# Kernel tuning notes

Hardware: AMD Instinct MI355X
Metric: run time of the kernel (lower is better)

The kernel has to match this reference:

```python
import jax, jax.numpy as jnp
import numpy as np

HEADS = 16
LN_EPS = 1e-5


def setup_inputs() -> dict:
    key = jax.random.key(0)
    ks = jax.random.split(key, 8)
    B, S, D = 2, 2048, 1024
    F = 4 * D
    std = 0.02
    return {
        "x": jax.random.normal(ks[0], (B, S, D), jnp.float32),
        # QKV projections (stored as (in, out)); kaiming-normal-like scale
        "Wq": jax.random.normal(ks[1], (D, D), jnp.float32) * std,
        "bq": jnp.zeros((D,), jnp.float32),
        "Wk": jax.random.normal(ks[2], (D, D), jnp.float32) * std,
        "bk": jnp.zeros((D,), jnp.float32),
        "Wv": jax.random.normal(ks[3], (D, D), jnp.float32) * std,
        "bv": jnp.zeros((D,), jnp.float32),
        # FFN
        "W1": jax.random.normal(ks[4], (D, F), jnp.float32) * std,
        "b1": jnp.zeros((F,), jnp.float32),
        "W2": jax.random.normal(ks[5], (F, D), jnp.float32) * std,
        "b2": jnp.zeros((D,), jnp.float32),
        # LayerNorm
        "gamma": jnp.ones((D,), jnp.float32),
        "beta": jnp.zeros((D,), jnp.float32),
    }


def reference(x, Wq, bq, Wk, bk, Wv, bv, W1, b1, W2, b2, gamma, beta):
    B, S, D = x.shape
    H = HEADS
    hd = D // H
    # QKV projections -> [B, H, S, hd]
    Q = (x @ Wq + bq).reshape(B, S, H, hd).transpose(0, 2, 1, 3)
    K = (x @ Wk + bk).reshape(B, S, H, hd).transpose(0, 2, 1, 3)
    V = (x @ Wv + bv).reshape(B, S, H, hd).transpose(0, 2, 1, 3)
    # scores scaled by sqrt(embedding_dim), faithful to source (not head_dim)
    scores = jnp.einsum('bhqd,bhkd->bhqk', Q, K) / jnp.sqrt(jnp.asarray(D, x.dtype))
    attn = jax.nn.softmax(scores, axis=-1)
    # diagonal_training: zero the diagonal of the post-softmax attention matrix
    attn = attn * (1.0 - jnp.eye(S, dtype=attn.dtype))
    out = jnp.einsum('bhqk,bhkd->bhqd', attn, V)
    out = out.transpose(0, 2, 1, 3).reshape(B, S, D)
    # dropout is identity in eval mode
    h = jax.nn.gelu(out @ W1 + b1, approximate=False) @ W2 + b2
    # LayerNorm
    mu = jnp.mean(h, axis=-1, keepdims=True)
    var = jnp.var(h, axis=-1, keepdims=True)
    return (h - mu) * jax.lax.rsqrt(var + LN_EPS) * gamma + beta
```

## Files before the change

kernel.cpp:

```cpp
#include <hip/hip_runtime.h>

using bf16x8 = __attribute__((ext_vector_type(8))) short;
using f32x4  = __attribute__((ext_vector_type(4))) float;

__device__ __forceinline__ float b2f(ushort u) {
  union { unsigned int i; float f; } v; v.i = ((unsigned int)u) << 16; return v.f;
}
__device__ __forceinline__ ushort f2b(float f) {
  unsigned int x = __float_as_uint(f);
  unsigned int r = (x + 0x7FFFu + ((x >> 16) & 1u)) >> 16;
  return (ushort)r;
}
__device__ __forceinline__ unsigned cvt_pk_bf16(float a, float b) {
  unsigned r;
  asm("v_cvt_pk_bf16_f32 %0, %1, %2" : "=v"(r) : "v"(a), "v"(b));
  return r;
}

__device__ __forceinline__ void gld_lds16(const void* g, void* l) {
  __builtin_amdgcn_global_load_lds(
      (const __attribute__((address_space(1))) void*)g,
      (__attribute__((address_space(3))) void*)l, 16, 0, 0);
}


__global__ void cast_bf16_kernel(const float* __restrict__ in, ushort* __restrict__ out, int n) {
  int i = (blockIdx.x * blockDim.x + threadIdx.x) * 4;
  if (i < n) {
    float4 v = *(const float4*)(in + i);
    ushort4 o = make_ushort4(f2b(v.x), f2b(v.y), f2b(v.z), f2b(v.w));
    *(ushort4*)(out + i) = o;
  }
}

__global__ void transpose_cast_kernel(const float* __restrict__ in, ushort* __restrict__ out,
                                      int R, int C) {
  __shared__ float tile[32][33];
  int tx = threadIdx.x, ty = threadIdx.y;
  int cb = blockIdx.x * 32, rb = blockIdx.y * 32;
  for (int i = ty; i < 32; i += 8)
    tile[i][tx] = in[(size_t)(rb + i) * C + (cb + tx)];
  __syncthreads();
  for (int i = ty; i < 32; i += 8)
    out[(size_t)(cb + i) * R + (rb + tx)] = f2b(tile[tx][i]);
}

__global__ void transpose_v_kernel(const ushort* __restrict__ V, ushort* __restrict__ Vt) {
  __shared__ ushort t[32][33];
  int bh = blockIdx.z;
  int s0 = blockIdx.x * 32, d0 = blockIdx.y * 32;
  const ushort* Vb = V + (size_t)bh * 2048 * 64;
  ushort* Vtb = Vt + (size_t)bh * 64 * 2048;
  int tx = threadIdx.x, ty = threadIdx.y;
  for (int i = ty; i < 32; i += 8) t[i][tx] = Vb[(size_t)(s0 + i) * 64 + d0 + tx];
  __syncthreads();
  for (int i = ty; i < 32; i += 8) Vtb[(size_t)(d0 + i) * 2048 + s0 + tx] = t[tx][i];
}


template<int EPI>
__global__ __launch_bounds__(512) void gemm256(
    const ushort* __restrict__ A, const ushort* __restrict__ Bt,
    const float* __restrict__ bias, void* __restrict__ Cout,
    int M, int N, int K)
{
  extern __shared__ ushort lds[];

  const int nwg = gridDim.x * gridDim.y;
  const int bid = blockIdx.y * gridDim.x + blockIdx.x;
  const int cpx = nwg >> 3;
  const int swz = (bid & 7) * cpx + (bid >> 3);
  const int bm = (swz % gridDim.x) * 256;
  const int bn = (swz / gridDim.x) * 256;

  const int tid = threadIdx.x;
  const int lane = tid & 63, w = tid >> 6;
  const int wr = w >> 2, wc = w & 3;
  const int g = lane >> 4, c = lane & 15;
  const int swz8 = ((g ^ (c & 3)) * 8);

  const int srow = tid >> 2;
  const int scol = (((tid & 3) ^ (srow & 3)) * 8);
  const ushort* gA = A  + (size_t)(bm + srow) * K + scol;
  const ushort* gB = Bt + (size_t)(bn + srow) * K + scol;
  const size_t rowK128 = (size_t)128 * K;

  const int NT = K / 32;
  f32x4 acc[8][4] = {};

  #pragma unroll
  for (int kt = 0; kt < 2; ++kt) {
    ushort* sA = &lds[kt * 16384];
    gld_lds16(gA + (size_t)kt * 32,            sA + tid * 8);
    gld_lds16(gA + rowK128 + (size_t)kt * 32,  sA + 4096 + tid * 8);
    gld_lds16(gB + (size_t)kt * 32,            sA + 8192 + tid * 8);
    gld_lds16(gB + rowK128 + (size_t)kt * 32,  sA + 8192 + 4096 + tid * 8);
  }

  for (int kt = 0; kt < NT; ++kt) {
    ushort* sA = &lds[(kt % 3) * 16384];
    ushort* sB = sA + 8192;
    const int stage_kt = kt + 2;
    ushort* sS = &lds[(stage_kt % 3) * 16384];

    __builtin_amdgcn_sched_barrier(0);
    if (kt + 1 < NT) asm volatile("s_waitcnt vmcnt(4)" ::: "memory");
    else             asm volatile("s_waitcnt vmcnt(0)" ::: "memory");
    __builtin_amdgcn_s_barrier();
    __builtin_amdgcn_sched_barrier(0);

    bf16x8 bf[4], af[4];
    #pragma unroll
    for (int n = 0; n < 4; ++n)
      bf[n] = *(const bf16x8*)&sB[(wc * 64 + n * 16 + c) * 32 + swz8];
    #pragma unroll
    for (int m = 0; m < 4; ++m)
      af[m] = *(const bf16x8*)&sA[(wr * 128 + m * 16 + c) * 32 + swz8];
    if (stage_kt < NT) {
      gld_lds16(gA + (size_t)stage_kt * 32,           sS + tid * 8);
      gld_lds16(gA + rowK128 + (size_t)stage_kt * 32, sS + 4096 + tid * 8);
    }
    asm volatile("s_waitcnt lgkmcnt(0)" ::: "memory");
    __builtin_amdgcn_sched_barrier(0);
    __builtin_amdgcn_s_setprio(1);
    #pragma unroll
    for (int m = 0; m < 4; ++m)
      #pragma unroll
      for (int n = 0; n < 4; ++n)
        acc[m][n] = __builtin_amdgcn_mfma_f32_16x16x32_bf16(af[m], bf[n], acc[m][n], 0, 0, 0);
    __builtin_amdgcn_s_setprio(0);
    __builtin_amdgcn_sched_barrier(0);

    #pragma unroll
    for (int m = 0; m < 4; ++m)
      af[m] = *(const bf16x8*)&sA[(wr * 128 + 64 + m * 16 + c) * 32 + swz8];
    if (stage_kt < NT) {
      gld_lds16(gB + (size_t)stage_kt * 32,           sS + 8192 + tid * 8);
      gld_lds16(gB + rowK128 + (size_t)stage_kt * 32, sS + 8192 + 4096 + tid * 8);
    }
    asm volatile("s_waitcnt lgkmcnt(0)" ::: "memory");
    __builtin_amdgcn_sched_barrier(0);
    __builtin_amdgcn_s_setprio(1);
    #pragma unroll
    for (int m = 0; m < 4; ++m)
      #pragma unroll
      for (int n = 0; n < 4; ++n)
        acc[4 + m][n] = __builtin_amdgcn_mfma_f32_16x16x32_bf16(af[m], bf[n], acc[4 + m][n], 0, 0, 0);
    __builtin_amdgcn_s_setprio(0);
    __builtin_amdgcn_sched_barrier(0);
  }

  #pragma unroll
  for (int n = 0; n < 4; ++n) {
    int col = bn + wc * 64 + n * 16 + c;
    float bia = bias[col];
    #pragma unroll
    for (int mf = 0; mf < 8; ++mf) {
      #pragma unroll
      for (int r = 0; r < 4; ++r) {
        int row = bm + wr * 128 + mf * 16 + g * 4 + r;
        float v = acc[mf][n][r] + bia;
        if (EPI == 1) {
          float u = 0.7978845608028654f * (v + 0.044715f * v * v * v);
          float au = fabsf(u);
          float e = __expf(-2.0f * au);
          float th = (1.0f - e) / (1.0f + e);
          th = copysignf(th, u);
          v = 0.5f * v * (1.0f + th);
          ((ushort*)Cout)[(size_t)row * N + col] = f2b(v);
        } else {
          int b = row >> 11, s = row & 2047;
          int which = col >> 10, cc = col & 1023;
          int hh = cc >> 6, d = cc & 63;
          ((ushort*)Cout)[(size_t)which * 4194304 +
                          ((size_t)((b * 16 + hh) * 2048 + s)) * 64 + d] = f2b(v);
        }
      }
    }
  }
}


#define BM 128
#define BN 128
#define BK 32

template<int EPI>
__global__ __launch_bounds__(256) void gemm_bf16(
    const ushort* __restrict__ A, const ushort* __restrict__ Bt,
    const float* __restrict__ bias, void* __restrict__ Cout, void* __restrict__ Cout2,
    int M, int N, int Kstride, int k_len)
{
  __shared__ ushort Asm_[2][BM * BK];
  __shared__ ushort Bsm_[2][BN * BK];
  const int bm = blockIdx.x * BM, bn = blockIdx.y * BN;
  const int k_begin = blockIdx.z * k_len;
  const int tid = threadIdx.x;
  const int lane = tid & 63, w = tid >> 6;
  const int wm = (w >> 1) * 64, wn = (w & 1) * 64;
  const int g = lane >> 4, c = lane & 15;
  const int srow = tid >> 2, scol = (tid & 3) * 8;
  const int soff = srow * 32 + scol;

  const ushort* gA0 = A  + (size_t)(bm + srow) * Kstride + k_begin + scol;
  const ushort* gA1 = gA0 + (size_t)64 * Kstride;
  const ushort* gB0 = Bt + (size_t)(bn + srow) * Kstride + k_begin + scol;
  const ushort* gB1 = gB0 + (size_t)64 * Kstride;

  f32x4 acc[4][4] = {};
  const int nt = k_len / BK;

  gld_lds16(gA0, &Asm_[0][soff]);
  gld_lds16(gA1, &Asm_[0][64 * 32 + soff]);
  gld_lds16(gB0, &Bsm_[0][soff]);
  gld_lds16(gB1, &Bsm_[0][64 * 32 + soff]);
  __syncthreads();

  int cur = 0;
  for (int t = 0; t < nt; ++t) {
    if (t + 1 < nt) {
      int k0 = (t + 1) * BK;
      gld_lds16(gA0 + k0, &Asm_[cur ^ 1][soff]);
      gld_lds16(gA1 + k0, &Asm_[cur ^ 1][64 * 32 + soff]);
      gld_lds16(gB0 + k0, &Bsm_[cur ^ 1][soff]);
      gld_lds16(gB1 + k0, &Bsm_[cur ^ 1][64 * 32 + soff]);
    }
    bf16x8 af[4], bfr[4];
    #pragma unroll
    for (int m = 0; m < 4; ++m)
      af[m] = *(const bf16x8*)&Asm_[cur][(wm + m * 16 + c) * 32 + g * 8];
    #pragma unroll
    for (int n = 0; n < 4; ++n)
      bfr[n] = *(const bf16x8*)&Bsm_[cur][(wn + n * 16 + c) * 32 + g * 8];
    #pragma unroll
    for (int m = 0; m < 4; ++m)
      #pragma unroll
      for (int n = 0; n < 4; ++n)
        acc[m][n] = __builtin_amdgcn_mfma_f32_16x16x32_bf16(af[m], bfr[n], acc[m][n], 0, 0, 0);
    __syncthreads();
    cur ^= 1;
  }

  #pragma unroll
  for (int n = 0; n < 4; ++n) {
    int col = bn + wn + n * 16 + c;
    float bia = bias ? bias[col] : 0.0f;
    #pragma unroll
    for (int m = 0; m < 4; ++m) {
      #pragma unroll
      for (int r = 0; r < 4; ++r) {
        int row = bm + wm + m * 16 + g * 4 + r;
        float v = acc[m][n][r] + bia;
        if (EPI == 2) {
          float* dst = (blockIdx.z == 0) ? (float*)Cout : (float*)Cout2;
          dst[(size_t)row * N + col] = v;
        } else {
          ((ushort*)Cout)[(size_t)row * N + col] = f2b(v);
        }
      }
    }
  }
}


#define ATT_SC2 0.0450842202f

__global__ __launch_bounds__(512) void attn_kernel(
    const ushort* __restrict__ Q, const ushort* __restrict__ K,
    const ushort* __restrict__ V, const ushort* __restrict__ Vt,
    ushort* __restrict__ Out)
{
  const int bh = blockIdx.y;
  const int b = bh >> 4, h = bh & 15;
  const int q0 = blockIdx.x * 128;
  const int tid = threadIdx.x;
  const int w = tid >> 6, lane = tid & 63;
  const int hi = lane >> 4, c = lane & 15;
  const int qw = q0 + w * 16;

  const ushort* Qb = Q + (size_t)bh * 2048 * 64;
  const ushort* Kb = K + (size_t)bh * 2048 * 64;
  const ushort* Vb = V + (size_t)bh * 2048 * 64;
  const ushort* Vtb = Vt + (size_t)bh * 64 * 2048;

  __shared__ ushort Ksm[2][64 * 64];
  __shared__ ushort Vsm[2][64 * 64];
  __shared__ ushort Psm[8][16 * 72];

  const int srow = tid >> 3;
  const int sslot = tid & 7;
  const int scolx = ((sslot ^ (srow & 7)) * 8);
  const ushort* gK = Kb + (size_t)srow * 64 + scolx;
  const ushort* gV = Vtb + (size_t)srow * 2048 + scolx;

  bf16x8 qf0 = *(const bf16x8*)(Qb + (size_t)(qw + c) * 64 + hi * 8);
  bf16x8 qf1 = *(const bf16x8*)(Qb + (size_t)(qw + c) * 64 + 32 + hi * 8);

  f32x4 acc[4] = {};
  float m_run = -1e30f, l_run = 0.f;

  gld_lds16(gK, &Ksm[0][tid * 8]);
  gld_lds16(gV, &Vsm[0][tid * 8]);
  __syncthreads();

  const int nt = 2048 / 64;
  for (int t = 0; t < nt; ++t) {
    const int buf = t & 1;
    if (t + 1 < nt) {
      gld_lds16(gK + (size_t)(t + 1) * 64 * 64, &Ksm[buf ^ 1][tid * 8]);
      gld_lds16(gV + (size_t)(t + 1) * 64,      &Vsm[buf ^ 1][tid * 8]);
    }

    f32x4 sv[4];
    #pragma unroll
    for (int sub = 0; sub < 4; ++sub) {
      int rr = sub * 16 + c;
      int sw = (rr & 7) * 8;
      bf16x8 k0 = *(const bf16x8*)&Ksm[buf][rr * 64 + ((hi * 8) ^ sw)];
      bf16x8 k1 = *(const bf16x8*)&Ksm[buf][rr * 64 + ((32 + hi * 8) ^ sw)];
      f32x4 z = {};
      __builtin_amdgcn_s_setprio(1);
      z = __builtin_amdgcn_mfma_f32_16x16x32_bf16(k0, qf0, z, 0, 0, 0);
      z = __builtin_amdgcn_mfma_f32_16x16x32_bf16(k1, qf1, z, 0, 0, 0);
      __builtin_amdgcn_s_setprio(0);
      #pragma unroll
      for (int r = 0; r < 4; ++r) sv[sub][r] = z[r] * ATT_SC2;
    }

    float tm = -1e30f;
    #pragma unroll
    for (int sub = 0; sub < 4; ++sub)
      #pragma unroll
      for (int r = 0; r < 4; ++r) tm = fmaxf(tm, sv[sub][r]);
    tm = fmaxf(tm, __shfl_xor(tm, 16));
    tm = fmaxf(tm, __shfl_xor(tm, 32));
    float mnew = fmaxf(m_run, tm);
    float p[16];
    float psum = 0.f;
    #pragma unroll
    for (int sub = 0; sub < 4; ++sub)
      #pragma unroll
      for (int r = 0; r < 4; ++r) { float e = exp2f(sv[sub][r] - mnew); p[sub * 4 + r] = e; psum += e; }
    psum += __shfl_xor(psum, 16);
    psum += __shfl_xor(psum, 32);
    float f = exp2f(m_run - mnew);
    l_run = l_run * f + psum;
    m_run = mnew;

    #pragma unroll
    for (int r = 0; r < 4; ++r) {
      float fr = __shfl(f, hi * 4 + r, 16);
      #pragma unroll
      for (int dsub = 0; dsub < 4; ++dsub) acc[dsub][r] *= fr;
    }

    #pragma unroll
    for (int sub = 0; sub < 4; ++sub) {
      uint2 pk;
      pk.x = cvt_pk_bf16(p[sub * 4 + 0], p[sub * 4 + 1]);
      pk.y = cvt_pk_bf16(p[sub * 4 + 2], p[sub * 4 + 3]);
      *(uint2*)&Psm[w][c * 72 + sub * 16 + hi * 4] = pk;
    }
    asm volatile("" ::: "memory");

    bf16x8 pa0 = *(const bf16x8*)&Psm[w][c * 72 + hi * 8];
    bf16x8 pa1 = *(const bf16x8*)&Psm[w][c * 72 + 32 + hi * 8];
    __builtin_amdgcn_s_setprio(1);
    #pragma unroll
    for (int dsub = 0; dsub < 4; ++dsub) {
      int rr = dsub * 16 + c;
      int sw = (rr & 7) * 8;
      bf16x8 v0 = *(const bf16x8*)&Vsm[buf][rr * 64 + ((hi * 8) ^ sw)];
      bf16x8 v1 = *(const bf16x8*)&Vsm[buf][rr * 64 + ((32 + hi * 8) ^ sw)];
      acc[dsub] = __builtin_amdgcn_mfma_f32_16x16x32_bf16(pa0, v0, acc[dsub], 0, 0, 0);
      acc[dsub] = __builtin_amdgcn_mfma_f32_16x16x32_bf16(pa1, v1, acc[dsub], 0, 0, 0);
    }
    __builtin_amdgcn_s_setprio(0);

    __syncthreads();
  }

  #pragma unroll
  for (int r = 0; r < 4; ++r) {
    int q = qw + hi * 4 + r;
    float part = 0.f;
    #pragma unroll
    for (int t = 0; t < 4; ++t)
      part += b2f(Qb[(size_t)q * 64 + c * 4 + t]) * b2f(Kb[(size_t)q * 64 + c * 4 + t]);
    #pragma unroll
    for (int off = 1; off < 16; off <<= 1) part += __shfl_xor(part, off);
    float mq = __shfl(m_run, hi * 4 + r, 16);
    float lq = __shfl(l_run, hi * 4 + r, 16);
    float pqq = exp2f(part * ATT_SC2 - mq);
    float inv = 1.f / lq;
    #pragma unroll
    for (int dsub = 0; dsub < 4; ++dsub) {
      float vq = b2f(Vb[(size_t)q * 64 + dsub * 16 + c]);
      float o = (acc[dsub][r] - pqq * vq) * inv;
      Out[((size_t)(b * 2048 + q) * 16 + h) * 64 + dsub * 16 + c] = f2b(o);
    }
  }
}


__global__ __launch_bounds__(256) void ln_kernel(float* __restrict__ h,
                                                 const float* __restrict__ p1,
                                                 const float* __restrict__ b2,
                                                 const float* __restrict__ gamma,
                                                 const float* __restrict__ beta) {
  int row = blockIdx.x, tid = threadIdx.x;
  float* hr = h + (size_t)row * 1024;
  const float* pr = p1 + (size_t)row * 1024;
  float4 v = ((const float4*)hr)[tid];
  float4 p = ((const float4*)pr)[tid];
  float4 bb = ((const float4*)b2)[tid];
  v.x += p.x + bb.x; v.y += p.y + bb.y; v.z += p.z + bb.z; v.w += p.w + bb.w;
  float s = v.x + v.y + v.z + v.w;
  #pragma unroll
  for (int off = 1; off < 64; off <<= 1) s += __shfl_xor(s, off);
  __shared__ float red[2][4];
  int wv = tid >> 6, lane = tid & 63;
  if (lane == 0) red[0][wv] = s;
  __syncthreads();
  float mu = (red[0][0] + red[0][1] + red[0][2] + red[0][3]) * (1.0f / 1024.0f);
  float dx = v.x - mu, dy = v.y - mu, dz = v.z - mu, dw = v.w - mu;
  float q = dx * dx + dy * dy + dz * dz + dw * dw;
  #pragma unroll
  for (int off = 1; off < 64; off <<= 1) q += __shfl_xor(q, off);
  if (lane == 0) red[1][wv] = q;
  __syncthreads();
  float var = (red[1][0] + red[1][1] + red[1][2] + red[1][3]) * (1.0f / 1024.0f);
  float is = rsqrtf(var + 1e-5f);
  float4 gm = ((const float4*)gamma)[tid];
  float4 bt = ((const float4*)beta)[tid];
  float4 o;
  o.x = dx * is * gm.x + bt.x;
  o.y = dy * is * gm.y + bt.y;
  o.z = dz * is * gm.z + bt.z;
  o.w = dw * is * gm.w + bt.w;
  ((float4*)hr)[tid] = o;
}


extern "C" void kernel_launch(void* const* d_in, const int* in_sizes, int n_in,
                              void* d_out, int out_size, void* d_ws, size_t ws_size,
                              hipStream_t stream) {
  const float* x  = (const float*)d_in[0];
  const float* Wq = (const float*)d_in[1];
  const float* bq = (const float*)d_in[2];
  const float* Wk = (const float*)d_in[3];
  const float* bk = (const float*)d_in[4];
  const float* Wv = (const float*)d_in[5];
  const float* bv = (const float*)d_in[6];
  const float* W1 = (const float*)d_in[7];
  const float* b1 = (const float*)d_in[8];
  const float* W2 = (const float*)d_in[9];
  const float* b2 = (const float*)d_in[10];
  const float* gamma = (const float*)d_in[11];
  const float* beta  = (const float*)d_in[12];
  float* out = (float*)d_out;

  char* ws = (char*)d_ws;
  const size_t MB = 1u << 20;
  ushort* xb    = (ushort*)(ws + 0);
  ushort* Wqkvt = (ushort*)(ws + 8 * MB);
  ushort* Qb    = (ushort*)(ws + 14 * MB);
  ushort* Kb    = (ushort*)(ws + 22 * MB);
  ushort* Vb    = (ushort*)(ws + 30 * MB);
  ushort* Vt    = (ushort*)(ws + 38 * MB);
  ushort* AO    = (ushort*)(ws + 46 * MB);
  ushort* W1t   = (ushort*)(ws + 0);
  ushort* h1    = (ushort*)(ws + 14 * MB);
  ushort* W2t   = (ushort*)(ws + 46 * MB);
  float*  p1    = (float*)(ws + 0);
  float*  bqkv  = (float*)(ws + 61 * MB);

  (void)hipMemcpyAsync(bqkv,        bq, 4096, hipMemcpyDeviceToDevice, stream);
  (void)hipMemcpyAsync(bqkv + 1024, bk, 4096, hipMemcpyDeviceToDevice, stream);
  (void)hipMemcpyAsync(bqkv + 2048, bv, 4096, hipMemcpyDeviceToDevice, stream);

  dim3 tb(32, 8);
  cast_bf16_kernel<<<4096, 256, 0, stream>>>(x, xb, 4194304);
  transpose_cast_kernel<<<dim3(32, 32), tb, 0, stream>>>(Wq, Wqkvt, 1024, 1024);
  transpose_cast_kernel<<<dim3(32, 32), tb, 0, stream>>>(Wk, Wqkvt + 1024 * 1024, 1024, 1024);
  transpose_cast_kernel<<<dim3(32, 32), tb, 0, stream>>>(Wv, Wqkvt + 2 * 1024 * 1024, 1024, 1024);

  gemm256<3><<<dim3(16, 12), 512, 98304, stream>>>(xb, Wqkvt, bqkv, Qb, 4096, 3072, 1024);

  transpose_cast_kernel<<<dim3(128, 32), tb, 0, stream>>>(W1, W1t, 1024, 4096);
  transpose_v_kernel<<<dim3(64, 2, 32), tb, 0, stream>>>(Vb, Vt);

  attn_kernel<<<dim3(16, 32), 512, 0, stream>>>(Qb, Kb, Vb, Vt, AO);

  gemm256<1><<<dim3(16, 16), 512, 98304, stream>>>(AO, W1t, b1, h1, 4096, 4096, 1024);

  transpose_cast_kernel<<<dim3(32, 128), tb, 0, stream>>>(W2, W2t, 4096, 1024);
  gemm_bf16<2><<<dim3(32, 8, 2), 256, 0, stream>>>(h1, W2t, nullptr, out, p1,
                                                   4096, 1024, 4096, 2048);

  ln_kernel<<<4096, 256, 0, stream>>>(out, p1, b2, gamma, beta);
}
```

Measured before the change: 264.6 us.

## Restage GEMM epilogues through LDS, change QKV layout, add split-K 4 for FFN2

The gemm256 epilogue now writes each fragment into a per-wave LDS staging buffer and then emits 16-byte row-contiguous global stores, replacing scattered 2-byte stores. The QKV output becomes a plain [B,S,D] layout, so the attention and V-transpose kernels now index with a 1024 stride. LDS swizzles are changed in both GEMMs to cut bank conflicts, and the second FFN GEMM gains a 4-way split-K when the workspace is large enough, with LayerNorm summing four partials. Weight transpose launches are also reordered and the workspace is remapped, which adds partial-sum traffic in exchange for more parallelism.

```diff
diff --git a/kernel.cpp b/kernel.cpp
--- a/kernel.cpp
+++ b/kernel.cpp
@@ -48,11 +48,12 @@
 __global__ void transpose_v_kernel(const ushort* __restrict__ V, ushort* __restrict__ Vt) {
   __shared__ ushort t[32][33];
   int bh = blockIdx.z;
+  int b = bh >> 4, h = bh & 15;
   int s0 = blockIdx.x * 32, d0 = blockIdx.y * 32;
-  const ushort* Vb = V + (size_t)bh * 2048 * 64;
+  const ushort* Vbp = V + ((size_t)b * 2048) * 1024 + h * 64;
   ushort* Vtb = Vt + (size_t)bh * 64 * 2048;
   int tx = threadIdx.x, ty = threadIdx.y;
-  for (int i = ty; i < 32; i += 8) t[i][tx] = Vb[(size_t)(s0 + i) * 64 + d0 + tx];
+  for (int i = ty; i < 32; i += 8) t[i][tx] = Vbp[(size_t)(s0 + i) * 1024 + d0 + tx];
   __syncthreads();
   for (int i = ty; i < 32; i += 8) Vtb[(size_t)(d0 + i) * 2048 + s0 + tx] = t[tx][i];
 }
@@ -77,10 +78,10 @@
   const int lane = tid & 63, w = tid >> 6;
   const int wr = w >> 2, wc = w & 3;
   const int g = lane >> 4, c = lane & 15;
-  const int swz8 = ((g ^ (c & 3)) * 8);
+  const int swz8 = ((g ^ ((c >> 1) & 3)) * 8);
 
   const int srow = tid >> 2;
-  const int scol = (((tid & 3) ^ (srow & 3)) * 8);
+  const int scol = (((tid & 3) ^ ((srow >> 1) & 3)) * 8);
   const ushort* gA = A  + (size_t)(bm + srow) * K + scol;
   const ushort* gB = Bt + (size_t)(bn + srow) * K + scol;
   const size_t rowK128 = (size_t)128 * K;
@@ -150,16 +151,21 @@
     __builtin_amdgcn_sched_barrier(0);
   }
 
-  #pragma unroll
-  for (int n = 0; n < 4; ++n) {
-    int col = bn + wc * 64 + n * 16 + c;
-    float bia = bias[col];
-    #pragma unroll
-    for (int mf = 0; mf < 8; ++mf) {
+  __syncthreads();
+  ushort* eb = &lds[w * 1088];
+  const int er = lane >> 3;
+  const int es = (lane & 7) * 8;
+  float bia[4];
+  #pragma unroll
+  for (int n = 0; n < 4; ++n) bia[n] = bias[bn + wc * 64 + n * 16 + c];
+
+  #pragma unroll
+  for (int mf = 0; mf < 8; ++mf) {
+    #pragma unroll
+    for (int n = 0; n < 4; ++n) {
       #pragma unroll
       for (int r = 0; r < 4; ++r) {
-        int row = bm + wr * 128 + mf * 16 + g * 4 + r;
-        float v = acc[mf][n][r] + bia;
+        float v = acc[mf][n][r] + bia[n];
         if (EPI == 1) {
           float u = 0.7978845608028654f * (v + 0.044715f * v * v * v);
           float au = fabsf(u);
@@ -167,16 +173,25 @@
           float th = (1.0f - e) / (1.0f + e);
           th = copysignf(th, u);
           v = 0.5f * v * (1.0f + th);
-          ((ushort*)Cout)[(size_t)row * N + col] = f2b(v);
-        } else {
-          int b = row >> 11, s = row & 2047;
-          int which = col >> 10, cc = col & 1023;
-          int hh = cc >> 6, d = cc & 63;
-          ((ushort*)Cout)[(size_t)which * 4194304 +
-                          ((size_t)((b * 16 + hh) * 2048 + s)) * 64 + d] = f2b(v);
         }
+        eb[(g * 4 + r) * 68 + n * 16 + c] = f2b(v);
       }
     }
+    asm volatile("" ::: "memory");
+    bf16x8 v0 = *(const bf16x8*)&eb[er * 68 + es];
+    bf16x8 v1 = *(const bf16x8*)&eb[(er + 8) * 68 + es];
+    int grow = bm + wr * 128 + mf * 16 + er;
+    int gcol = bn + wc * 64 + es;
+    if (EPI == 3) {
+      ushort* dst = (ushort*)Cout + (size_t)(gcol >> 10) * 4194304 + (gcol & 1023);
+      *(bf16x8*)(dst + (size_t)grow * 1024) = v0;
+      *(bf16x8*)(dst + (size_t)(grow + 8) * 1024) = v1;
+    } else {
+      ushort* dst = (ushort*)Cout + gcol;
+      *(bf16x8*)(dst + (size_t)grow * N) = v0;
+      *(bf16x8*)(dst + (size_t)(grow + 8) * N) = v1;
+    }
+    asm volatile("" ::: "memory");
   }
 }
 
@@ -185,10 +200,10 @@
 #define BN 128
 #define BK 32
 
-template<int EPI>
-__global__ __launch_bounds__(256) void gemm_bf16(
+__global__ __launch_bounds__(256) void gemm_bf16_f32(
     const ushort* __restrict__ A, const ushort* __restrict__ Bt,
-    const float* __restrict__ bias, void* __restrict__ Cout, void* __restrict__ Cout2,
+    float* __restrict__ C0, float* __restrict__ C1,
+    float* __restrict__ C2, float* __restrict__ C3,
     int M, int N, int Kstride, int k_len)
 {
   __shared__ ushort Asm_[2][BM * BK];
@@ -199,8 +214,10 @@
   const int lane = tid & 63, w = tid >> 6;
   const int wm = (w >> 1) * 64, wn = (w & 1) * 64;
   const int g = lane >> 4, c = lane & 15;
-  const int srow = tid >> 2, scol = (tid & 3) * 8;
-  const int soff = srow * 32 + scol;
+  const int swz8 = ((g ^ ((c >> 1) & 3)) * 8);
+  const int srow = tid >> 2;
+  const int scol = (((tid & 3) ^ ((srow >> 1) & 3)) * 8);
+  const int soff = srow * 32 + (tid & 3) * 8;
 
   const ushort* gA0 = A  + (size_t)(bm + srow) * Kstride + k_begin + scol;
   const ushort* gA1 = gA0 + (size_t)64 * Kstride;
@@ -228,10 +245,10 @@
     bf16x8 af[4], bfr[4];
     #pragma unroll
     for (int m = 0; m < 4; ++m)
-      af[m] = *(const bf16x8*)&Asm_[cur][(wm + m * 16 + c) * 32 + g * 8];
+      af[m] = *(const bf16x8*)&Asm_[cur][(wm + m * 16 + c) * 32 + swz8];
     #pragma unroll
     for (int n = 0; n < 4; ++n)
-      bfr[n] = *(const bf16x8*)&Bsm_[cur][(wn + n * 16 + c) * 32 + g * 8];
+      bfr[n] = *(const bf16x8*)&Bsm_[cur][(wn + n * 16 + c) * 32 + swz8];
     #pragma unroll
     for (int m = 0; m < 4; ++m)
       #pragma unroll
@@ -241,24 +258,21 @@
     cur ^= 1;
   }
 
+  float* dst = C0;
+  if (blockIdx.z == 1) dst = C1;
+  else if (blockIdx.z == 2) dst = C2;
+  else if (blockIdx.z == 3) dst = C3;
+
   #pragma unroll
   for (int n = 0; n < 4; ++n) {
     int col = bn + wn + n * 16 + c;
-    float bia = bias ? bias[col] : 0.0f;
-    #pragma unroll
-    for (int m = 0; m < 4; ++m) {
+    #pragma unroll
+    for (int m = 0; m < 4; ++m)
       #pragma unroll
       for (int r = 0; r < 4; ++r) {
         int row = bm + wm + m * 16 + g * 4 + r;
-        float v = acc[m][n][r] + bia;
-        if (EPI == 2) {
-          float* dst = (blockIdx.z == 0) ? (float*)Cout : (float*)Cout2;
-          dst[(size_t)row * N + col] = v;
-        } else {
-          ((ushort*)Cout)[(size_t)row * N + col] = f2b(v);
-        }
+        dst[(size_t)row * N + col] = acc[m][n][r];
       }
-    }
   }
 }
 
@@ -278,9 +292,10 @@
   const int hi = lane >> 4, c = lane & 15;
   const int qw = q0 + w * 16;
 
-  const ushort* Qb = Q + (size_t)bh * 2048 * 64;
-  const ushort* Kb = K + (size_t)bh * 2048 * 64;
-  const ushort* Vb = V + (size_t)bh * 2048 * 64;
+  const size_t boff = ((size_t)b * 2048) * 1024 + h * 64;
+  const ushort* Qp = Q + boff;
+  const ushort* Kp = K + boff;
+  const ushort* Vp = V + boff;
   const ushort* Vtb = Vt + (size_t)bh * 64 * 2048;
 
   __shared__ ushort Ksm[2][64 * 64];
@@ -290,11 +305,11 @@
   const int srow = tid >> 3;
   const int sslot = tid & 7;
   const int scolx = ((sslot ^ (srow & 7)) * 8);
-  const ushort* gK = Kb + (size_t)srow * 64 + scolx;
+  const ushort* gK = Kp + (size_t)srow * 1024 + scolx;
   const ushort* gV = Vtb + (size_t)srow * 2048 + scolx;
 
-  bf16x8 qf0 = *(const bf16x8*)(Qb + (size_t)(qw + c) * 64 + hi * 8);
-  bf16x8 qf1 = *(const bf16x8*)(Qb + (size_t)(qw + c) * 64 + 32 + hi * 8);
+  bf16x8 qf0 = *(const bf16x8*)(Qp + (size_t)(qw + c) * 1024 + hi * 8);
+  bf16x8 qf1 = *(const bf16x8*)(Qp + (size_t)(qw + c) * 1024 + 32 + hi * 8);
 
   f32x4 acc[4] = {};
   float m_run = -1e30f, l_run = 0.f;
@@ -307,8 +322,8 @@
   for (int t = 0; t < nt; ++t) {
     const int buf = t & 1;
     if (t + 1 < nt) {
-      gld_lds16(gK + (size_t)(t + 1) * 64 * 64, &Ksm[buf ^ 1][tid * 8]);
-      gld_lds16(gV + (size_t)(t + 1) * 64,      &Vsm[buf ^ 1][tid * 8]);
+      gld_lds16(gK + (size_t)(t + 1) * 64 * 1024, &Ksm[buf ^ 1][tid * 8]);
+      gld_lds16(gV + (size_t)(t + 1) * 64,        &Vsm[buf ^ 1][tid * 8]);
     }
 
     f32x4 sv[4];
@@ -386,7 +401,7 @@
     float part = 0.f;
     #pragma unroll
     for (int t = 0; t < 4; ++t)
-      part += b2f(Qb[(size_t)q * 64 + c * 4 + t]) * b2f(Kb[(size_t)q * 64 + c * 4 + t]);
+      part += b2f(Qp[(size_t)q * 1024 + c * 4 + t]) * b2f(Kp[(size_t)q * 1024 + c * 4 + t]);
     #pragma unroll
     for (int off = 1; off < 16; off <<= 1) part += __shfl_xor(part, off);
     float mq = __shfl(m_run, hi * 4 + r, 16);
@@ -395,7 +410,7 @@
     float inv = 1.f / lq;
     #pragma unroll
     for (int dsub = 0; dsub < 4; ++dsub) {
-      float vq = b2f(Vb[(size_t)q * 64 + dsub * 16 + c]);
+      float vq = b2f(Vp[(size_t)q * 1024 + dsub * 16 + c]);
       float o = (acc[dsub][r] - pqq * vq) * inv;
       Out[((size_t)(b * 2048 + q) * 16 + h) * 64 + dsub * 16 + c] = f2b(o);
     }
@@ -405,16 +420,22 @@
 
 __global__ __launch_bounds__(256) void ln_kernel(float* __restrict__ h,
                                                  const float* __restrict__ p1,
+                                                 const float* __restrict__ p2,
+                                                 const float* __restrict__ p3,
                                                  const float* __restrict__ b2,
                                                  const float* __restrict__ gamma,
-                                                 const float* __restrict__ beta) {
+                                                 const float* __restrict__ beta, int np) {
   int row = blockIdx.x, tid = threadIdx.x;
   float* hr = h + (size_t)row * 1024;
-  const float* pr = p1 + (size_t)row * 1024;
   float4 v = ((const float4*)hr)[tid];
-  float4 p = ((const float4*)pr)[tid];
+  float4 p = ((const float4*)(p1 + (size_t)row * 1024))[tid];
   float4 bb = ((const float4*)b2)[tid];
   v.x += p.x + bb.x; v.y += p.y + bb.y; v.z += p.z + bb.z; v.w += p.w + bb.w;
+  if (np == 4) {
+    float4 a = ((const float4*)(p2 + (size_t)row * 1024))[tid];
+    float4 d = ((const float4*)(p3 + (size_t)row * 1024))[tid];
+    v.x += a.x + d.x; v.y += a.y + d.y; v.z += a.z + d.z; v.w += a.w + d.w;
+  }
   float s = v.x + v.y + v.z + v.w;
   #pragma unroll
   for (int off = 1; off < 64; off <<= 1) s += __shfl_xor(s, off);
@@ -469,11 +490,15 @@
   ushort* Vb    = (ushort*)(ws + 30 * MB);
   ushort* Vt    = (ushort*)(ws + 38 * MB);
   ushort* AO    = (ushort*)(ws + 46 * MB);
-  ushort* W1t   = (ushort*)(ws + 0);
-  ushort* h1    = (ushort*)(ws + 14 * MB);
-  ushort* W2t   = (ushort*)(ws + 46 * MB);
-  float*  p1    = (float*)(ws + 0);
-  float*  bqkv  = (float*)(ws + 61 * MB);
+  ushort* W1t   = (ushort*)(ws + 54 * MB);
+  ushort* h1    = (ushort*)(ws + 0);
+  ushort* W2t   = (ushort*)(ws + 32 * MB);
+  float*  p1    = (float*)(ws + 40 * MB);
+  float*  p2    = (float*)(ws + 56 * MB);
+  float*  p3    = (float*)(ws + 72 * MB);
+  float*  bqkv  = (float*)(ws + 46 * MB);
+
+  const bool split4 = (ws_size >= (size_t)89 * MB);
 
   (void)hipMemcpyAsync(bqkv,        bq, 4096, hipMemcpyDeviceToDevice, stream);
   (void)hipMemcpyAsync(bqkv + 1024, bk, 4096, hipMemcpyDeviceToDevice, stream);
@@ -484,19 +509,25 @@
   transpose_cast_kernel<<<dim3(32, 32), tb, 0, stream>>>(Wq, Wqkvt, 1024, 1024);
   transpose_cast_kernel<<<dim3(32, 32), tb, 0, stream>>>(Wk, Wqkvt + 1024 * 1024, 1024, 1024);
   transpose_cast_kernel<<<dim3(32, 32), tb, 0, stream>>>(Wv, Wqkvt + 2 * 1024 * 1024, 1024, 1024);
+  transpose_cast_kernel<<<dim3(128, 32), tb, 0, stream>>>(W1, W1t, 1024, 4096);
 
   gemm256<3><<<dim3(16, 12), 512, 98304, stream>>>(xb, Wqkvt, bqkv, Qb, 4096, 3072, 1024);
 
-  transpose_cast_kernel<<<dim3(128, 32), tb, 0, stream>>>(W1, W1t, 1024, 4096);
   transpose_v_kernel<<<dim3(64, 2, 32), tb, 0, stream>>>(Vb, Vt);
 
   attn_kernel<<<dim3(16, 32), 512, 0, stream>>>(Qb, Kb, Vb, Vt, AO);
 
+  transpose_cast_kernel<<<dim3(32, 128), tb, 0, stream>>>(W2, W2t, 4096, 1024);
+
   gemm256<1><<<dim3(16, 16), 512, 98304, stream>>>(AO, W1t, b1, h1, 4096, 4096, 1024);
 
-  transpose_cast_kernel<<<dim3(32, 128), tb, 0, stream>>>(W2, W2t, 4096, 1024);
-  gemm_bf16<2><<<dim3(32, 8, 2), 256, 0, stream>>>(h1, W2t, nullptr, out, p1,
-                                                   4096, 1024, 4096, 2048);
-
-  ln_kernel<<<4096, 256, 0, stream>>>(out, p1, b2, gamma, beta);
-}
+  if (split4) {
+    gemm_bf16_f32<<<dim3(32, 8, 4), 256, 0, stream>>>(h1, W2t, out, p1, p2, p3,
+                                                      4096, 1024, 4096, 1024);
+    ln_kernel<<<4096, 256, 0, stream>>>(out, p1, p2, p3, b2, gamma, beta, 4);
+  } else {
+    gemm_bf16_f32<<<dim3(32, 8, 2), 256, 0, stream>>>(h1, W2t, out, p1, nullptr, nullptr,
+                                                      4096, 1024, 4096, 2048);
+    ln_kernel<<<4096, 256, 0, stream>>>(out, p1, nullptr, nullptr, b2, gamma, beta, 2);
+  }
+}
```

New measurement: 253.1 us. 4.3% less time.
